# Optimization experiments

Measured on AMD Instinct MI355X. Metric: run time of the kernel, lower is better.

Reference implementation:

```python
import jax, jax.numpy as jnp
import numpy as np

N = 100_000          # total nodes across batch
E = 3_200_000        # total edges
L = 64               # token sequence length per node
VOCAB = 6
EMBED = 16
HID = 16             # gcn_hidden
EDGE_FEAT = 5
EDGE_HID = 16
NUM_GRAPHS = 64
NODE_IN = EMBED + 1  # Hseq concat x_cov


def setup_inputs() -> dict:
    key = jax.random.key(0)
    ks = jax.random.split(key, 14)
    seq_tokens = jax.random.randint(ks[0], (N, L), 0, VOCAB, dtype=jnp.int32)
    x_cov = jax.random.normal(ks[1], (N, 1), dtype=jnp.float32)
    edge_index = jax.random.randint(ks[2], (2, E), 0, N, dtype=jnp.int32)
    edge_attr = jax.random.normal(ks[3], (E, EDGE_FEAT), dtype=jnp.float32)
    batch = jnp.sort(jax.random.randint(ks[4], (N,), 0, NUM_GRAPHS, dtype=jnp.int32))
    # parameters
    embed = jax.random.normal(ks[5], (VOCAB, EMBED), dtype=jnp.float32) * 0.1
    embed = embed.at[0].set(0.0)  # padding_idx=0
    w1 = jax.random.normal(ks[6], (NODE_IN, HID), dtype=jnp.float32) * (NODE_IN ** -0.5)
    b1 = jnp.zeros((HID,), jnp.float32)
    w2 = jax.random.normal(ks[7], (HID, HID), dtype=jnp.float32) * (HID ** -0.5)
    b2 = jnp.zeros((HID,), jnp.float32)
    we1 = jax.random.normal(ks[8], (2 * HID + EDGE_FEAT, EDGE_HID), dtype=jnp.float32) * ((2 * HID + EDGE_FEAT) ** -0.5)
    be1 = jnp.zeros((EDGE_HID,), jnp.float32)
    we2 = jax.random.normal(ks[9], (EDGE_HID, 1), dtype=jnp.float32) * (EDGE_HID ** -0.5)
    be2 = jnp.zeros((1,), jnp.float32)
    return dict(seq_tokens=seq_tokens, x_cov=x_cov, edge_index=edge_index,
                edge_attr=edge_attr, batch=batch, embed=embed,
                w1=w1, b1=b1, w2=w2, b2=b2, we1=we1, be1=be1, we2=we2, be2=be2)


def reference(seq_tokens, x_cov, edge_index, edge_attr, batch,
              embed, w1, b1, w2, b2, we1, be1, we2, be2):
    # --- encode_nodes: masked mean of token embeddings + covariate ---
    Emb = embed[seq_tokens]                                   # [N, L, EMBED]
    mask = (seq_tokens != 0).astype(jnp.float32)[..., None]   # [N, L, 1]
    lengths = jnp.maximum(mask.sum(axis=1), 1.0)              # [N, 1]
    Hseq = (Emb * mask).sum(axis=1) / lengths                 # [N, EMBED]
    X = jnp.concatenate([Hseq, x_cov], axis=1)                # [N, NODE_IN]

    # --- per-graph dense GCN, expressed as equivalent block-diagonal sparse MP ---
    src, dst = edge_index[0], edge_index[1]
    valid = (batch[src] == batch[dst]).astype(jnp.float32)    # within-graph edges only
    # row-sum degree: out-degree (valid edges) + self loop + eps, per torch code
    deg = jax.ops.segment_sum(valid, src, num_segments=N) + 1.0 + 1e-8
    dinv = deg ** -0.5                                        # [N]

    def gcn(H, W, b):
        M = H @ W + b                                         # [N, HID]
        msg = (valid * dinv[dst])[:, None] * M[dst]           # [E, HID]
        agg = jax.ops.segment_sum(msg, src, num_segments=N)   # scatter-add over src
        return jax.nn.relu(dinv[:, None] * (agg + dinv[:, None] * M))

    H = gcn(X, w1, b1)
    H = gcn(H, w2, b2)

    # --- edge MLP on gathered node pairs ---
    feats = jnp.concatenate([H[src], H[dst], edge_attr], axis=1)  # [E, 2*HID+5]
    h = jax.nn.relu(feats @ we1 + be1)
    logits = (h @ we2 + be2)[:, 0]                            # [E]
    return logits
```

## Files before the change

### kernel.cpp

```cpp
#include <hip/hip_runtime.h>
#include <hip/hip_bf16.h>
#include <hip/hip_fp16.h>

#define BS 256
#define NG 64
#define VCAP 131072
#define PBUF 256

__device__ __forceinline__ uint4 pack8(const float* f) {
    union { uint4 u; __half2 h[4]; } v;
    v.h[0] = __floats2half2_rn(f[0], f[1]);
    v.h[1] = __floats2half2_rn(f[2], f[3]);
    v.h[2] = __floats2half2_rn(f[4], f[5]);
    v.h[3] = __floats2half2_rn(f[6], f[7]);
    return v.u;
}

__device__ __forceinline__ void unpack8(uint4 u, float* f) {
    const __half2* h = (const __half2*)&u;
    float2 t;
    t = __half22float2(h[0]); f[0] = t.x; f[1] = t.y;
    t = __half22float2(h[1]); f[2] = t.x; f[3] = t.y;
    t = __half22float2(h[2]); f[4] = t.x; f[5] = t.y;
    t = __half22float2(h[3]); f[6] = t.x; f[7] = t.y;
}

__global__ __launch_bounds__(BS) void encode_kernel(
        const int* __restrict__ seq,
        const float* __restrict__ xcov,
        const int* __restrict__ batch,
        const float* __restrict__ embed,
        const float* __restrict__ w1,
        const float* __restrict__ b1,
        float* __restrict__ M1,
        int* __restrict__ deg,
        int* __restrict__ tail,
        int* __restrict__ bnd, int N) {
    __shared__ float sE[96];
    __shared__ float sW1[272];
    __shared__ float sB1[16];
    __shared__ float sEW[80];
    int tid = threadIdx.x;
    for (int i = tid; i < 96; i += BS) sE[i] = embed[i];
    for (int i = tid; i < 272; i += BS) sW1[i] = w1[i];
    if (tid < 16) sB1[tid] = b1[tid];
    __syncthreads();
    if (tid < 80) {
        int t = tid >> 4, j = tid & 15;
        float a = 0.f;
#pragma unroll
        for (int k = 0; k < 16; k++) a += sE[(t + 1) * 16 + k] * sW1[k * 16 + j];
        sEW[tid] = a;
    }
    __syncthreads();

    int gid = blockIdx.x * BS + tid;
    if (gid < N) deg[gid] = 0;
    if (gid == 0) *tail = 0;

    int n = blockIdx.x * 16 + (tid >> 4);
    int j = tid & 15;
    if (n >= N) return;

    if (j == 0) {
        int b = batch[n];
        if (n == 0) {
            for (int g = 0; g <= b; g++) bnd[g] = 0;
        } else {
            int pb = batch[n - 1];
            for (int g = pb + 1; g <= b; g++) bnd[g] = n;
        }
        if (n == N - 1) {
            for (int g = b + 1; g <= NG; g++) bnd[g] = N;
        }
    }

    int4 v = ((const int4*)seq)[(size_t)n * 16 + j];
    int c1 = (v.x == 1) + (v.y == 1) + (v.z == 1) + (v.w == 1);
    int c2 = (v.x == 2) + (v.y == 2) + (v.z == 2) + (v.w == 2);
    int c3 = (v.x == 3) + (v.y == 3) + (v.z == 3) + (v.w == 3);
    int c4 = (v.x == 4) + (v.y == 4) + (v.z == 4) + (v.w == 4);
    int c5 = (v.x == 5) + (v.y == 5) + (v.z == 5) + (v.w == 5);
#pragma unroll
    for (int m = 1; m < 16; m <<= 1) {
        c1 += __shfl_xor(c1, m);
        c2 += __shfl_xor(c2, m);
        c3 += __shfl_xor(c3, m);
        c4 += __shfl_xor(c4, m);
        c5 += __shfl_xor(c5, m);
    }
    float f1 = (float)c1, f2 = (float)c2, f3 = (float)c3, f4 = (float)c4, f5 = (float)c5;
    float tot = f1 + f2 + f3 + f4 + f5;
    float inv = 1.0f / fmaxf(tot, 1.0f);
    float xc = xcov[n];
    float o = sB1[j] + xc * sW1[256 + j] +
              inv * (f1 * sEW[j] + f2 * sEW[16 + j] + f3 * sEW[32 + j] +
                     f4 * sEW[48 + j] + f5 * sEW[64 + j]);
    M1[(size_t)n * 16 + j] = o;
}

__device__ __forceinline__ int find_graph(const int* bnd, int s) {
    int g = 0;
#pragma unroll
    for (int step = 32; step; step >>= 1) {
        int c = g + step;
        if (c <= NG - 1 && bnd[c] <= s) g = c;
    }
    return g;
}

__global__ __launch_bounds__(BS) void prep_kernel(
        const int* __restrict__ ei,
        const int* __restrict__ bndg,
        int* __restrict__ deg,
        int2* __restrict__ vlist,
        int* __restrict__ tail, int E) {
    __shared__ int sBnd[NG + 1];
    __shared__ int2 sList[PBUF];
    __shared__ int sCnt;
    __shared__ int sBase;
    int tid = threadIdx.x;
    if (tid <= NG) sBnd[tid] = bndg[tid];
    if (tid == 0) sCnt = 0;
    __syncthreads();

    int idx = (blockIdx.x * BS + tid) * 4;
    if (idx + 3 < E) {
        int4 s4 = *(const int4*)(ei + idx);
        int4 d4 = *(const int4*)(ei + E + idx);
#pragma unroll
        for (int j = 0; j < 4; j++) {
            int s = (&s4.x)[j], d = (&d4.x)[j];
            int g = find_graph(sBnd, s);
            if (d >= sBnd[g] && d < sBnd[g + 1]) {
                atomicAdd(&deg[s], 1);
                int lp = atomicAdd(&sCnt, 1);
                if (lp < PBUF) sList[lp] = make_int2(s, d);
            }
        }
    } else {
        for (int j = 0; j < 4; j++) {
            int e = idx + j;
            if (e < E) {
                int s = ei[e], d = ei[E + e];
                int g = find_graph(sBnd, s);
                if (d >= sBnd[g] && d < sBnd[g + 1]) {
                    atomicAdd(&deg[s], 1);
                    int lp = atomicAdd(&sCnt, 1);
                    if (lp < PBUF) sList[lp] = make_int2(s, d);
                }
            }
        }
    }
    __syncthreads();
    if (tid == 0) {
        int c = sCnt < PBUF ? sCnt : PBUF;
        sBase = atomicAdd(tail, c);
        sCnt = c;
    }
    __syncthreads();
    int c = sCnt, b = sBase;
    for (int i = tid; i < c; i += BS) {
        int gp = b + i;
        if (gp < VCAP) vlist[gp] = sList[i];
    }
}

__global__ __launch_bounds__(BS) void scan1_kernel(
        const int* __restrict__ deg,
        int* __restrict__ off,
        int* __restrict__ bsum,
        int* __restrict__ csrD, int N) {
    __shared__ int wsum[4];
    int tid = threadIdx.x;
    int n = blockIdx.x * BS + tid;

    int stride = gridDim.x * BS;
    for (int i = blockIdx.x * BS + tid; i < VCAP; i += stride) csrD[i] = 0;

    int v = (n < N) ? deg[n] : 0;
    int lane = tid & 63, wv = tid >> 6;
    int x = v;
#pragma unroll
    for (int o = 1; o < 64; o <<= 1) {
        int y = __shfl_up(x, o);
        if (lane >= o) x += y;
    }
    if (lane == 63) wsum[wv] = x;
    __syncthreads();
    if (wv == 0 && lane < 4) {
        int w = wsum[lane];
#pragma unroll
        for (int o = 1; o < 4; o <<= 1) {
            int y = __shfl_up(w, o);
            if (lane >= o) w += y;
        }
        wsum[lane] = w;
    }
    __syncthreads();
    int base = (wv > 0) ? wsum[wv - 1] : 0;
    if (n < N) off[n] = base + x - v;
    if (tid == BS - 1) bsum[blockIdx.x] = wsum[3];
}

__global__ __launch_bounds__(64) void scan2_kernel(int* __restrict__ bsum, int nb) {
    int lane = threadIdx.x;
    int l[8];
    int s = 0;
    int base0 = lane * 8;
#pragma unroll
    for (int k = 0; k < 8; k++) {
        int i = base0 + k;
        l[k] = (i < nb) ? bsum[i] : 0;
        s += l[k];
    }
    int x = s;
#pragma unroll
    for (int o = 1; o < 64; o <<= 1) {
        int y = __shfl_up(x, o);
        if (lane >= o) x += y;
    }
    int run = x - s;
#pragma unroll
    for (int k = 0; k < 8; k++) {
        int i = base0 + k;
        if (i < nb) bsum[i] = run;
        run += l[k];
    }
}

__global__ __launch_bounds__(BS) void scan3_kernel(
        const int* __restrict__ deg,
        const int* __restrict__ off,
        const int* __restrict__ bsum,
        int2* __restrict__ OD,
        int* __restrict__ cur,
        float* __restrict__ Dinv, int N) {
    int n = blockIdx.x * BS + threadIdx.x;
    if (n >= N) return;
    int beg = off[n] + bsum[blockIdx.x];
    int dg = deg[n];
    OD[n] = make_int2(beg, dg);
    cur[n] = beg;
    Dinv[n] = 1.0f / sqrtf((float)dg + 1.0f + 1e-8f);
}

__global__ __launch_bounds__(BS) void place_kernel(
        const int2* __restrict__ vlist,
        const int* __restrict__ tail,
        int* __restrict__ cur,
        int* __restrict__ csrD) {
    int nt = *tail;
    if (nt > VCAP) nt = VCAP;
    int stride = gridDim.x * BS;
    for (int i = blockIdx.x * BS + threadIdx.x; i < nt; i += stride) {
        int2 e = vlist[i];
        int pos = atomicAdd(&cur[e.x], 1);
        if (pos < VCAP) csrD[pos] = e.y;
    }
}

__global__ __launch_bounds__(BS) void layer1_kernel(
        const int2* __restrict__ OD,
        const float* __restrict__ Dinv,
        const int* __restrict__ csrD,
        const float* __restrict__ M1,
        float* __restrict__ M2,
        const float* __restrict__ w2,
        const float* __restrict__ b2,
        int N) {
    __shared__ float sW2[256];
    __shared__ float sB2[16];
    int tid = threadIdx.x;
    for (int i = tid; i < 256; i += BS) sW2[i] = w2[i];
    if (tid < 16) sB2[tid] = b2[tid];
    __syncthreads();

    int n = blockIdx.x * BS + tid;
    if (n >= N) return;

    int2 od = OD[n];
    float di = Dinv[n];
    float acc[16];
#pragma unroll
    for (int j = 0; j < 16; j++) acc[j] = 0.f;
    int beg = od.x, end = od.x + od.y;
    if (beg > VCAP) beg = VCAP;
    if (end > VCAP) end = VCAP;
    for (int e = beg; e < end; e++) {
        int d = csrD[e];
        float dd = Dinv[d];
        const float4* m4 = (const float4*)(M1 + (size_t)d * 16);
        float4 a = m4[0], b = m4[1], c = m4[2], q = m4[3];
        acc[0] += dd * a.x; acc[1] += dd * a.y; acc[2] += dd * a.z; acc[3] += dd * a.w;
        acc[4] += dd * b.x; acc[5] += dd * b.y; acc[6] += dd * b.z; acc[7] += dd * b.w;
        acc[8] += dd * c.x; acc[9] += dd * c.y; acc[10] += dd * c.z; acc[11] += dd * c.w;
        acc[12] += dd * q.x; acc[13] += dd * q.y; acc[14] += dd * q.z; acc[15] += dd * q.w;
    }
    const float4* mr = (const float4*)(M1 + (size_t)n * 16);
    float4 m0 = mr[0], m1 = mr[1], m2 = mr[2], m3 = mr[3];
    float m[16] = {m0.x,m0.y,m0.z,m0.w, m1.x,m1.y,m1.z,m1.w,
                   m2.x,m2.y,m2.z,m2.w, m3.x,m3.y,m3.z,m3.w};
    float h[16];
#pragma unroll
    for (int j = 0; j < 16; j++) h[j] = fmaxf(di * (acc[j] + di * m[j]), 0.0f);
    float o[16];
#pragma unroll
    for (int j = 0; j < 16; j++) o[j] = sB2[j];
#pragma unroll
    for (int k = 0; k < 16; k++) {
        float hk = h[k];
#pragma unroll
        for (int j = 0; j < 16; j++) o[j] += hk * sW2[k * 16 + j];
    }
    float4* wr = (float4*)(M2 + (size_t)n * 16);
    wr[0] = make_float4(o[0], o[1], o[2], o[3]);
    wr[1] = make_float4(o[4], o[5], o[6], o[7]);
    wr[2] = make_float4(o[8], o[9], o[10], o[11]);
    wr[3] = make_float4(o[12], o[13], o[14], o[15]);
}

__global__ __launch_bounds__(BS) void layer2_kernel(
        const int2* __restrict__ OD,
        const float* __restrict__ Dinv,
        const int* __restrict__ csrD,
        const float* __restrict__ M2,
        char* __restrict__ PQ,
        const float* __restrict__ we1,
        int N) {
    __shared__ float sWe1[512];
    int tid = threadIdx.x;
    for (int i = tid; i < 512; i += BS) sWe1[i] = we1[i];
    __syncthreads();

    int n = blockIdx.x * BS + tid;
    if (n >= N) return;

    int2 od = OD[n];
    float di = Dinv[n];
    float acc[16];
#pragma unroll
    for (int j = 0; j < 16; j++) acc[j] = 0.f;
    int beg = od.x, end = od.x + od.y;
    if (beg > VCAP) beg = VCAP;
    if (end > VCAP) end = VCAP;
    for (int e = beg; e < end; e++) {
        int d = csrD[e];
        float dd = Dinv[d];
        const float4* m4 = (const float4*)(M2 + (size_t)d * 16);
        float4 a = m4[0], b = m4[1], c = m4[2], q = m4[3];
        acc[0] += dd * a.x; acc[1] += dd * a.y; acc[2] += dd * a.z; acc[3] += dd * a.w;
        acc[4] += dd * b.x; acc[5] += dd * b.y; acc[6] += dd * b.z; acc[7] += dd * b.w;
        acc[8] += dd * c.x; acc[9] += dd * c.y; acc[10] += dd * c.z; acc[11] += dd * c.w;
        acc[12] += dd * q.x; acc[13] += dd * q.y; acc[14] += dd * q.z; acc[15] += dd * q.w;
    }
    const float4* mr = (const float4*)(M2 + (size_t)n * 16);
    float4 m0 = mr[0], m1 = mr[1], m2 = mr[2], m3 = mr[3];
    float m[16] = {m0.x,m0.y,m0.z,m0.w, m1.x,m1.y,m1.z,m1.w,
                   m2.x,m2.y,m2.z,m2.w, m3.x,m3.y,m3.z,m3.w};
    float h[16];
#pragma unroll
    for (int j = 0; j < 16; j++) h[j] = fmaxf(di * (acc[j] + di * m[j]), 0.0f);
    float p[16], q[16];
#pragma unroll
    for (int j = 0; j < 16; j++) { p[j] = 0.f; q[j] = 0.f; }
#pragma unroll
    for (int k = 0; k < 16; k++) {
        float hk = h[k];
#pragma unroll
        for (int j = 0; j < 16; j++) {
            p[j] += hk * sWe1[k * 16 + j];
            q[j] += hk * sWe1[(16 + k) * 16 + j];
        }
    }
    uint4* pr = (uint4*)(PQ + (size_t)n * 64);
    pr[0] = pack8(p); pr[1] = pack8(p + 8);
    pr[2] = pack8(q); pr[3] = pack8(q + 8);
}

__device__ __forceinline__ float mlp_one(
        uint4 pa, uint4 pb, uint4 qa, uint4 qb,
        float a0, float a1, float a2, float a3, float a4,
        const float* sB, const float* sC, const float* sV, float sb2) {
    float p[16], q[16];
    unpack8(pa, p); unpack8(pb, p + 8);
    unpack8(qa, q); unpack8(qb, q + 8);
    float lg = sb2;
#pragma unroll
    for (int j = 0; j < 16; j++) {
        float acc = sB[j] + p[j] + q[j] +
                    a0 * sC[j] + a1 * sC[16 + j] + a2 * sC[32 + j] +
                    a3 * sC[48 + j] + a4 * sC[64 + j];
        lg += fmaxf(acc, 0.0f) * sV[j];
    }
    return lg;
}

__global__ __launch_bounds__(BS) void edge_mlp_kernel(
        const int* __restrict__ ei,
        const char* __restrict__ PQ,
        const float* __restrict__ eattr,
        const float* __restrict__ we1,
        const float* __restrict__ be1,
        const float* __restrict__ we2,
        const float* __restrict__ be2,
        float* __restrict__ out, int E) {
    __shared__ float sC[80];
    __shared__ float sB[16];
    __shared__ float sV[16];
    __shared__ float sb2;
    int tid = threadIdx.x;
    if (tid < 80) sC[tid] = we1[512 + tid];
    if (tid < 16) { sB[tid] = be1[tid]; sV[tid] = we2[tid]; }
    if (tid == 0) sb2 = be2[0];
    __syncthreads();

    int e0 = (blockIdx.x * BS + tid) * 4;
    if (e0 >= E) return;

    if (e0 + 3 < E) {
        int4 s4 = *(const int4*)(ei + e0);
        int4 d4 = *(const int4*)(ei + E + e0);
        const uint4* p0 = (const uint4*)(PQ + (size_t)s4.x * 64);
        const uint4* p1 = (const uint4*)(PQ + (size_t)s4.y * 64);
        const uint4* p2 = (const uint4*)(PQ + (size_t)s4.z * 64);
        const uint4* p3 = (const uint4*)(PQ + (size_t)s4.w * 64);
        const uint4* q0 = (const uint4*)(PQ + (size_t)d4.x * 64 + 32);
        const uint4* q1 = (const uint4*)(PQ + (size_t)d4.y * 64 + 32);
        const uint4* q2 = (const uint4*)(PQ + (size_t)d4.z * 64 + 32);
        const uint4* q3 = (const uint4*)(PQ + (size_t)d4.w * 64 + 32);
        uint4 pa0 = p0[0], pb0 = p0[1], qa0 = q0[0], qb0 = q0[1];
        uint4 pa1 = p1[0], pb1 = p1[1], qa1 = q1[0], qb1 = q1[1];
        uint4 pa2 = p2[0], pb2 = p2[1], qa2 = q2[0], qb2 = q2[1];
        uint4 pa3 = p3[0], pb3 = p3[1], qa3 = q3[0], qb3 = q3[1];
        const float4* at = (const float4*)(eattr + (size_t)e0 * 5);
        float4 A0 = at[0], A1 = at[1], A2 = at[2], A3 = at[3], A4 = at[4];

        float r0 = mlp_one(pa0, pb0, qa0, qb0, A0.x, A0.y, A0.z, A0.w, A1.x, sB, sC, sV, sb2);
        float r1 = mlp_one(pa1, pb1, qa1, qb1, A1.y, A1.z, A1.w, A2.x, A2.y, sB, sC, sV, sb2);
        float r2 = mlp_one(pa2, pb2, qa2, qb2, A2.z, A2.w, A3.x, A3.y, A3.z, sB, sC, sV, sb2);
        float r3 = mlp_one(pa3, pb3, qa3, qb3, A3.w, A4.x, A4.y, A4.z, A4.w, sB, sC, sV, sb2);
        *(float4*)(out + e0) = make_float4(r0, r1, r2, r3);
    } else {
        for (int j = 0; j < 4; j++) {
            int e = e0 + j;
            if (e < E) {
                int s = ei[e], d = ei[E + e];
                const uint4* pr = (const uint4*)(PQ + (size_t)s * 64);
                const uint4* qr = (const uint4*)(PQ + (size_t)d * 64 + 32);
                uint4 pa = pr[0], pb = pr[1], qa = qr[0], qb = qr[1];
                const float* ea = eattr + (size_t)e * 5;
                float lg = mlp_one(pa, pb, qa, qb, ea[0], ea[1], ea[2], ea[3], ea[4],
                                   sB, sC, sV, sb2);
                out[e] = lg;
            }
        }
    }
}

extern "C" void kernel_launch(void* const* d_in, const int* in_sizes, int n_in,
                              void* d_out, int out_size, void* d_ws, size_t ws_size,
                              hipStream_t stream) {
    const int* seq     = (const int*)d_in[0];
    const float* xcov  = (const float*)d_in[1];
    const int* ei      = (const int*)d_in[2];
    const float* eattr = (const float*)d_in[3];
    const int* batch   = (const int*)d_in[4];
    const float* embed = (const float*)d_in[5];
    const float* w1    = (const float*)d_in[6];
    const float* b1    = (const float*)d_in[7];
    const float* w2    = (const float*)d_in[8];
    const float* b2    = (const float*)d_in[9];
    const float* we1   = (const float*)d_in[10];
    const float* be1   = (const float*)d_in[11];
    const float* we2   = (const float*)d_in[12];
    const float* be2   = (const float*)d_in[13];
    float* out         = (float*)d_out;

    int N = in_sizes[1];
    int E = in_sizes[2] / 2;

    char* ws = (char*)d_ws;
    size_t off_b = 0;
    auto alloc = [&](size_t bytes) -> void* {
        void* p = ws + off_b;
        off_b += (bytes + 255) & ~(size_t)255;
        return p;
    };
    float* M1    = (float*)alloc((size_t)N * 16 * sizeof(float));
    float* M2    = (float*)alloc((size_t)N * 16 * sizeof(float));
    char* PQ     = (char*)alloc((size_t)N * 64);
    int* bndg    = (int*)alloc((NG + 1) * sizeof(int));
    int* deg     = (int*)alloc((size_t)N * sizeof(int));
    int* offA    = (int*)alloc((size_t)N * sizeof(int));
    int* cur     = (int*)alloc((size_t)N * sizeof(int));
    int2* OD     = (int2*)alloc((size_t)N * sizeof(int2));
    float* Dinv  = (float*)alloc((size_t)N * sizeof(float));
    int* bsum    = (int*)alloc(512 * sizeof(int));
    int2* vlist  = (int2*)alloc((size_t)VCAP * sizeof(int2));
    int* csrD    = (int*)alloc((size_t)VCAP * sizeof(int));
    int* tail    = (int*)alloc(16 * sizeof(int));

    int gn16 = ((size_t)N * 16 + BS - 1) / BS;
    int gp   = (E + BS * 4 - 1) / (BS * 4);
    int gs   = (N + BS - 1) / BS;
    int ge4  = (E + BS * 4 - 1) / (BS * 4);

    encode_kernel<<<gn16, BS, 0, stream>>>(seq, xcov, batch, embed, w1, b1,
                                           M1, deg, tail, bndg, N);
    prep_kernel<<<gp, BS, 0, stream>>>(ei, bndg, deg, vlist, tail, E);
    scan1_kernel<<<gs, BS, 0, stream>>>(deg, offA, bsum, csrD, N);
    scan2_kernel<<<1, 64, 0, stream>>>(bsum, gs);
    scan3_kernel<<<gs, BS, 0, stream>>>(deg, offA, bsum, OD, cur, Dinv, N);
    place_kernel<<<208, BS, 0, stream>>>(vlist, tail, cur, csrD);
    layer1_kernel<<<gs, BS, 0, stream>>>(OD, Dinv, csrD, M1, M2, w2, b2, N);
    layer2_kernel<<<gs, BS, 0, stream>>>(OD, Dinv, csrD, M2, PQ, we1, N);
    edge_mlp_kernel<<<ge4, BS, 0, stream>>>(ei, PQ, eattr, we1, be1, we2, be2, out, E);
}
```

Measured before the change: 301.3 us.

## Replace CSR build with atomic scatter aggregation and per-feature node kernels

Drops the scan and place kernels that built a CSR of valid edges. Aggregation becomes an atomic scatter-add of dinv-scaled neighbor features into zeroed accumulators A1 and A2. Node layers now run 16 threads per node and broadcast features with shuffles, and the edge MLP goes to one edge per thread with nontemporal loads. The aim is fewer launches and less serial scan work, at the cost of float atomics, extra zeroing traffic and nondeterministic summation order.

Result: faster. 290.4 us (-3.6%).

```diff
diff --git a/kernel.cpp b/kernel.cpp
--- a/kernel.cpp
+++ b/kernel.cpp
@@ -33,6 +33,8 @@
         const float* __restrict__ w1,
         const float* __restrict__ b1,
         float* __restrict__ M1,
+        float* __restrict__ A1,
+        float* __restrict__ A2,
         int* __restrict__ deg,
         int* __restrict__ tail,
         int* __restrict__ bnd, int N) {
@@ -54,8 +56,9 @@
     }
     __syncthreads();
 
-    int gid = blockIdx.x * BS + tid;
-    if (gid < N) deg[gid] = 0;
+    size_t gid = (size_t)blockIdx.x * BS + tid;
+    if (gid < (size_t)N * 16) { A1[gid] = 0.f; A2[gid] = 0.f; }
+    if (gid < (size_t)N) deg[gid] = 0;
     if (gid == 0) *tail = 0;
 
     int n = blockIdx.x * 16 + (tid >> 4);
@@ -166,109 +169,31 @@
     }
 }
 
-__global__ __launch_bounds__(BS) void scan1_kernel(
-        const int* __restrict__ deg,
-        int* __restrict__ off,
-        int* __restrict__ bsum,
-        int* __restrict__ csrD, int N) {
-    __shared__ int wsum[4];
-    int tid = threadIdx.x;
-    int n = blockIdx.x * BS + tid;
-
-    int stride = gridDim.x * BS;
-    for (int i = blockIdx.x * BS + tid; i < VCAP; i += stride) csrD[i] = 0;
-
-    int v = (n < N) ? deg[n] : 0;
-    int lane = tid & 63, wv = tid >> 6;
-    int x = v;
-#pragma unroll
-    for (int o = 1; o < 64; o <<= 1) {
-        int y = __shfl_up(x, o);
-        if (lane >= o) x += y;
-    }
-    if (lane == 63) wsum[wv] = x;
-    __syncthreads();
-    if (wv == 0 && lane < 4) {
-        int w = wsum[lane];
-#pragma unroll
-        for (int o = 1; o < 4; o <<= 1) {
-            int y = __shfl_up(w, o);
-            if (lane >= o) w += y;
-        }
-        wsum[lane] = w;
-    }
-    __syncthreads();
-    int base = (wv > 0) ? wsum[wv - 1] : 0;
-    if (n < N) off[n] = base + x - v;
-    if (tid == BS - 1) bsum[blockIdx.x] = wsum[3];
-}
-
-__global__ __launch_bounds__(64) void scan2_kernel(int* __restrict__ bsum, int nb) {
-    int lane = threadIdx.x;
-    int l[8];
-    int s = 0;
-    int base0 = lane * 8;
-#pragma unroll
-    for (int k = 0; k < 8; k++) {
-        int i = base0 + k;
-        l[k] = (i < nb) ? bsum[i] : 0;
-        s += l[k];
-    }
-    int x = s;
-#pragma unroll
-    for (int o = 1; o < 64; o <<= 1) {
-        int y = __shfl_up(x, o);
-        if (lane >= o) x += y;
-    }
-    int run = x - s;
-#pragma unroll
-    for (int k = 0; k < 8; k++) {
-        int i = base0 + k;
-        if (i < nb) bsum[i] = run;
-        run += l[k];
-    }
-}
-
-__global__ __launch_bounds__(BS) void scan3_kernel(
-        const int* __restrict__ deg,
-        const int* __restrict__ off,
-        const int* __restrict__ bsum,
-        int2* __restrict__ OD,
-        int* __restrict__ cur,
-        float* __restrict__ Dinv, int N) {
-    int n = blockIdx.x * BS + threadIdx.x;
-    if (n >= N) return;
-    int beg = off[n] + bsum[blockIdx.x];
-    int dg = deg[n];
-    OD[n] = make_int2(beg, dg);
-    cur[n] = beg;
-    Dinv[n] = 1.0f / sqrtf((float)dg + 1.0f + 1e-8f);
-}
-
-__global__ __launch_bounds__(BS) void place_kernel(
+__global__ __launch_bounds__(BS) void scatter_kernel(
         const int2* __restrict__ vlist,
         const int* __restrict__ tail,
-        int* __restrict__ cur,
-        int* __restrict__ csrD) {
+        const int* __restrict__ deg,
+        const float* __restrict__ M,
+        float* __restrict__ A) {
     int nt = *tail;
     if (nt > VCAP) nt = VCAP;
-    int stride = gridDim.x * BS;
-    for (int i = blockIdx.x * BS + threadIdx.x; i < nt; i += stride) {
+    int j = threadIdx.x & 15;
+    int estep = gridDim.x * (BS / 16);
+    for (int i = blockIdx.x * (BS / 16) + (threadIdx.x >> 4); i < nt; i += estep) {
         int2 e = vlist[i];
-        int pos = atomicAdd(&cur[e.x], 1);
-        if (pos < VCAP) csrD[pos] = e.y;
-    }
-}
-
-__global__ __launch_bounds__(BS) void layer1_kernel(
-        const int2* __restrict__ OD,
-        const float* __restrict__ Dinv,
-        const int* __restrict__ csrD,
+        float dd = 1.0f / sqrtf((float)deg[e.y] + 1.0f + 1e-8f);
+        float val = dd * M[(size_t)e.y * 16 + j];
+        atomicAdd(&A[(size_t)e.x * 16 + j], val);
+    }
+}
+
+__global__ __launch_bounds__(BS) void finish1_kernel(
+        const float* __restrict__ A1,
         const float* __restrict__ M1,
-        float* __restrict__ M2,
+        const int* __restrict__ deg,
         const float* __restrict__ w2,
         const float* __restrict__ b2,
-        int N) {
+        float* __restrict__ M2, int N) {
     __shared__ float sW2[256];
     __shared__ float sB2[16];
     int tid = threadIdx.x;
@@ -276,124 +201,58 @@
     if (tid < 16) sB2[tid] = b2[tid];
     __syncthreads();
 
-    int n = blockIdx.x * BS + tid;
+    int n = blockIdx.x * 16 + (tid >> 4);
+    int j = tid & 15;
     if (n >= N) return;
 
-    int2 od = OD[n];
-    float di = Dinv[n];
-    float acc[16];
-#pragma unroll
-    for (int j = 0; j < 16; j++) acc[j] = 0.f;
-    int beg = od.x, end = od.x + od.y;
-    if (beg > VCAP) beg = VCAP;
-    if (end > VCAP) end = VCAP;
-    for (int e = beg; e < end; e++) {
-        int d = csrD[e];
-        float dd = Dinv[d];
-        const float4* m4 = (const float4*)(M1 + (size_t)d * 16);
-        float4 a = m4[0], b = m4[1], c = m4[2], q = m4[3];
-        acc[0] += dd * a.x; acc[1] += dd * a.y; acc[2] += dd * a.z; acc[3] += dd * a.w;
-        acc[4] += dd * b.x; acc[5] += dd * b.y; acc[6] += dd * b.z; acc[7] += dd * b.w;
-        acc[8] += dd * c.x; acc[9] += dd * c.y; acc[10] += dd * c.z; acc[11] += dd * c.w;
-        acc[12] += dd * q.x; acc[13] += dd * q.y; acc[14] += dd * q.z; acc[15] += dd * q.w;
-    }
-    const float4* mr = (const float4*)(M1 + (size_t)n * 16);
-    float4 m0 = mr[0], m1 = mr[1], m2 = mr[2], m3 = mr[3];
-    float m[16] = {m0.x,m0.y,m0.z,m0.w, m1.x,m1.y,m1.z,m1.w,
-                   m2.x,m2.y,m2.z,m2.w, m3.x,m3.y,m3.z,m3.w};
-    float h[16];
-#pragma unroll
-    for (int j = 0; j < 16; j++) h[j] = fmaxf(di * (acc[j] + di * m[j]), 0.0f);
-    float o[16];
-#pragma unroll
-    for (int j = 0; j < 16; j++) o[j] = sB2[j];
+    float di = 1.0f / sqrtf((float)deg[n] + 1.0f + 1e-8f);
+    size_t base = (size_t)n * 16;
+    float a = A1[base + j];
+    float m = M1[base + j];
+    float h = fmaxf(di * (a + di * m), 0.0f);
+
+    int lb = (tid & 63) & 48;
+    float o = sB2[j];
 #pragma unroll
     for (int k = 0; k < 16; k++) {
-        float hk = h[k];
-#pragma unroll
-        for (int j = 0; j < 16; j++) o[j] += hk * sW2[k * 16 + j];
-    }
-    float4* wr = (float4*)(M2 + (size_t)n * 16);
-    wr[0] = make_float4(o[0], o[1], o[2], o[3]);
-    wr[1] = make_float4(o[4], o[5], o[6], o[7]);
-    wr[2] = make_float4(o[8], o[9], o[10], o[11]);
-    wr[3] = make_float4(o[12], o[13], o[14], o[15]);
-}
-
-__global__ __launch_bounds__(BS) void layer2_kernel(
-        const int2* __restrict__ OD,
-        const float* __restrict__ Dinv,
-        const int* __restrict__ csrD,
+        float hk = __shfl(h, lb + k);
+        o += hk * sW2[k * 16 + j];
+    }
+    M2[base + j] = o;
+}
+
+__global__ __launch_bounds__(BS) void finish2_kernel(
+        const float* __restrict__ A2,
         const float* __restrict__ M2,
-        char* __restrict__ PQ,
+        const int* __restrict__ deg,
         const float* __restrict__ we1,
-        int N) {
+        char* __restrict__ PQ, int N) {
     __shared__ float sWe1[512];
     int tid = threadIdx.x;
     for (int i = tid; i < 512; i += BS) sWe1[i] = we1[i];
     __syncthreads();
 
-    int n = blockIdx.x * BS + tid;
+    int n = blockIdx.x * 16 + (tid >> 4);
+    int j = tid & 15;
     if (n >= N) return;
 
-    int2 od = OD[n];
-    float di = Dinv[n];
-    float acc[16];
-#pragma unroll
-    for (int j = 0; j < 16; j++) acc[j] = 0.f;
-    int beg = od.x, end = od.x + od.y;
-    if (beg > VCAP) beg = VCAP;
-    if (end > VCAP) end = VCAP;
-    for (int e = beg; e < end; e++) {
-        int d = csrD[e];
-        float dd = Dinv[d];
-        const float4* m4 = (const float4*)(M2 + (size_t)d * 16);
-        float4 a = m4[0], b = m4[1], c = m4[2], q = m4[3];
-        acc[0] += dd * a.x; acc[1] += dd * a.y; acc[2] += dd * a.z; acc[3] += dd * a.w;
-        acc[4] += dd * b.x; acc[5] += dd * b.y; acc[6] += dd * b.z; acc[7] += dd * b.w;
-        acc[8] += dd * c.x; acc[9] += dd * c.y; acc[10] += dd * c.z; acc[11] += dd * c.w;
-        acc[12] += dd * q.x; acc[13] += dd * q.y; acc[14] += dd * q.z; acc[15] += dd * q.w;
-    }
-    const float4* mr = (const float4*)(M2 + (size_t)n * 16);
-    float4 m0 = mr[0], m1 = mr[1], m2 = mr[2], m3 = mr[3];
-    float m[16] = {m0.x,m0.y,m0.z,m0.w, m1.x,m1.y,m1.z,m1.w,
-                   m2.x,m2.y,m2.z,m2.w, m3.x,m3.y,m3.z,m3.w};
-    float h[16];
-#pragma unroll
-    for (int j = 0; j < 16; j++) h[j] = fmaxf(di * (acc[j] + di * m[j]), 0.0f);
-    float p[16], q[16];
-#pragma unroll
-    for (int j = 0; j < 16; j++) { p[j] = 0.f; q[j] = 0.f; }
+    float di = 1.0f / sqrtf((float)deg[n] + 1.0f + 1e-8f);
+    size_t base = (size_t)n * 16;
+    float a = A2[base + j];
+    float m = M2[base + j];
+    float h = fmaxf(di * (a + di * m), 0.0f);
+
+    int lb = (tid & 63) & 48;
+    float p = 0.f, q = 0.f;
 #pragma unroll
     for (int k = 0; k < 16; k++) {
-        float hk = h[k];
-#pragma unroll
-        for (int j = 0; j < 16; j++) {
-            p[j] += hk * sWe1[k * 16 + j];
-            q[j] += hk * sWe1[(16 + k) * 16 + j];
-        }
-    }
-    uint4* pr = (uint4*)(PQ + (size_t)n * 64);
-    pr[0] = pack8(p); pr[1] = pack8(p + 8);
-    pr[2] = pack8(q); pr[3] = pack8(q + 8);
-}
-
-__device__ __forceinline__ float mlp_one(
-        uint4 pa, uint4 pb, uint4 qa, uint4 qb,
-        float a0, float a1, float a2, float a3, float a4,
-        const float* sB, const float* sC, const float* sV, float sb2) {
-    float p[16], q[16];
-    unpack8(pa, p); unpack8(pb, p + 8);
-    unpack8(qa, q); unpack8(qb, q + 8);
-    float lg = sb2;
-#pragma unroll
-    for (int j = 0; j < 16; j++) {
-        float acc = sB[j] + p[j] + q[j] +
-                    a0 * sC[j] + a1 * sC[16 + j] + a2 * sC[32 + j] +
-                    a3 * sC[48 + j] + a4 * sC[64 + j];
-        lg += fmaxf(acc, 0.0f) * sV[j];
-    }
-    return lg;
+        float hk = __shfl(h, lb + k);
+        p += hk * sWe1[k * 16 + j];
+        q += hk * sWe1[(16 + k) * 16 + j];
+    }
+    __half* row = (__half*)(PQ + (size_t)n * 64);
+    row[j] = __float2half(p);
+    row[16 + j] = __float2half(q);
 }
 
 __global__ __launch_bounds__(BS) void edge_mlp_kernel(
@@ -414,48 +273,34 @@
     if (tid < 16) { sB[tid] = be1[tid]; sV[tid] = we2[tid]; }
     if (tid == 0) sb2 = be2[0];
     __syncthreads();
-
-    int e0 = (blockIdx.x * BS + tid) * 4;
-    if (e0 >= E) return;
-
-    if (e0 + 3 < E) {
-        int4 s4 = *(const int4*)(ei + e0);
-        int4 d4 = *(const int4*)(ei + E + e0);
-        const uint4* p0 = (const uint4*)(PQ + (size_t)s4.x * 64);
-        const uint4* p1 = (const uint4*)(PQ + (size_t)s4.y * 64);
-        const uint4* p2 = (const uint4*)(PQ + (size_t)s4.z * 64);
-        const uint4* p3 = (const uint4*)(PQ + (size_t)s4.w * 64);
-        const uint4* q0 = (const uint4*)(PQ + (size_t)d4.x * 64 + 32);
-        const uint4* q1 = (const uint4*)(PQ + (size_t)d4.y * 64 + 32);
-        const uint4* q2 = (const uint4*)(PQ + (size_t)d4.z * 64 + 32);
-        const uint4* q3 = (const uint4*)(PQ + (size_t)d4.w * 64 + 32);
-        uint4 pa0 = p0[0], pb0 = p0[1], qa0 = q0[0], qb0 = q0[1];
-        uint4 pa1 = p1[0], pb1 = p1[1], qa1 = q1[0], qb1 = q1[1];
-        uint4 pa2 = p2[0], pb2 = p2[1], qa2 = q2[0], qb2 = q2[1];
-        uint4 pa3 = p3[0], pb3 = p3[1], qa3 = q3[0], qb3 = q3[1];
-        const float4* at = (const float4*)(eattr + (size_t)e0 * 5);
-        float4 A0 = at[0], A1 = at[1], A2 = at[2], A3 = at[3], A4 = at[4];
-
-        float r0 = mlp_one(pa0, pb0, qa0, qb0, A0.x, A0.y, A0.z, A0.w, A1.x, sB, sC, sV, sb2);
-        float r1 = mlp_one(pa1, pb1, qa1, qb1, A1.y, A1.z, A1.w, A2.x, A2.y, sB, sC, sV, sb2);
-        float r2 = mlp_one(pa2, pb2, qa2, qb2, A2.z, A2.w, A3.x, A3.y, A3.z, sB, sC, sV, sb2);
-        float r3 = mlp_one(pa3, pb3, qa3, qb3, A3.w, A4.x, A4.y, A4.z, A4.w, sB, sC, sV, sb2);
-        *(float4*)(out + e0) = make_float4(r0, r1, r2, r3);
-    } else {
-        for (int j = 0; j < 4; j++) {
-            int e = e0 + j;
-            if (e < E) {
-                int s = ei[e], d = ei[E + e];
-                const uint4* pr = (const uint4*)(PQ + (size_t)s * 64);
-                const uint4* qr = (const uint4*)(PQ + (size_t)d * 64 + 32);
-                uint4 pa = pr[0], pb = pr[1], qa = qr[0], qb = qr[1];
-                const float* ea = eattr + (size_t)e * 5;
-                float lg = mlp_one(pa, pb, qa, qb, ea[0], ea[1], ea[2], ea[3], ea[4],
-                                   sB, sC, sV, sb2);
-                out[e] = lg;
-            }
-        }
-    }
+    int e = blockIdx.x * BS + tid;
+    if (e >= E) return;
+    int s = __builtin_nontemporal_load(ei + e);
+    int d = __builtin_nontemporal_load(ei + E + e);
+    const uint4* pr = (const uint4*)(PQ + (size_t)s * 64);
+    const uint4* qr = (const uint4*)(PQ + (size_t)d * 64 + 32);
+    uint4 pa = pr[0], pb = pr[1];
+    uint4 qa = qr[0], qb = qr[1];
+    const float* ea = eattr + (size_t)e * 5;
+    float a0 = __builtin_nontemporal_load(ea + 0);
+    float a1 = __builtin_nontemporal_load(ea + 1);
+    float a2 = __builtin_nontemporal_load(ea + 2);
+    float a3 = __builtin_nontemporal_load(ea + 3);
+    float a4 = __builtin_nontemporal_load(ea + 4);
+
+    float p[16], q[16];
+    unpack8(pa, p); unpack8(pb, p + 8);
+    unpack8(qa, q); unpack8(qb, q + 8);
+
+    float lg = sb2;
+#pragma unroll
+    for (int j = 0; j < 16; j++) {
+        float acc = sB[j] + p[j] + q[j] +
+                    a0 * sC[j] + a1 * sC[16 + j] + a2 * sC[32 + j] +
+                    a3 * sC[48 + j] + a4 * sC[64 + j];
+        lg += fmaxf(acc, 0.0f) * sV[j];
+    }
+    __builtin_nontemporal_store(lg, out + e);
 }
 
 extern "C" void kernel_launch(void* const* d_in, const int* in_sizes, int n_in,
@@ -489,31 +334,24 @@
     };
     float* M1    = (float*)alloc((size_t)N * 16 * sizeof(float));
     float* M2    = (float*)alloc((size_t)N * 16 * sizeof(float));
+    float* A1    = (float*)alloc((size_t)N * 16 * sizeof(float));
+    float* A2    = (float*)alloc((size_t)N * 16 * sizeof(float));
     char* PQ     = (char*)alloc((size_t)N * 64);
     int* bndg    = (int*)alloc((NG + 1) * sizeof(int));
     int* deg     = (int*)alloc((size_t)N * sizeof(int));
-    int* offA    = (int*)alloc((size_t)N * sizeof(int));
-    int* cur     = (int*)alloc((size_t)N * sizeof(int));
-    int2* OD     = (int2*)alloc((size_t)N * sizeof(int2));
-    float* Dinv  = (float*)alloc((size_t)N * sizeof(float));
-    int* bsum    = (int*)alloc(512 * sizeof(int));
     int2* vlist  = (int2*)alloc((size_t)VCAP * sizeof(int2));
-    int* csrD    = (int*)alloc((size_t)VCAP * sizeof(int));
     int* tail    = (int*)alloc(16 * sizeof(int));
 
-    int gn16 = ((size_t)N * 16 + BS - 1) / BS;
+    int gn16 = (int)(((size_t)N * 16 + BS - 1) / BS);
     int gp   = (E + BS * 4 - 1) / (BS * 4);
-    int gs   = (N + BS - 1) / BS;
-    int ge4  = (E + BS * 4 - 1) / (BS * 4);
+    int ge   = (E + BS - 1) / BS;
 
     encode_kernel<<<gn16, BS, 0, stream>>>(seq, xcov, batch, embed, w1, b1,
-                                           M1, deg, tail, bndg, N);
+                                           M1, A1, A2, deg, tail, bndg, N);
     prep_kernel<<<gp, BS, 0, stream>>>(ei, bndg, deg, vlist, tail, E);
-    scan1_kernel<<<gs, BS, 0, stream>>>(deg, offA, bsum, csrD, N);
-    scan2_kernel<<<1, 64, 0, stream>>>(bsum, gs);
-    scan3_kernel<<<gs, BS, 0, stream>>>(deg, offA, bsum, OD, cur, Dinv, N);
-    place_kernel<<<208, BS, 0, stream>>>(vlist, tail, cur, csrD);
-    layer1_kernel<<<gs, BS, 0, stream>>>(OD, Dinv, csrD, M1, M2, w2, b2, N);
-    layer2_kernel<<<gs, BS, 0, stream>>>(OD, Dinv, csrD, M2, PQ, we1, N);
-    edge_mlp_kernel<<<ge4, BS, 0, stream>>>(ei, PQ, eattr, we1, be1, we2, be2, out, E);
-}
+    scatter_kernel<<<1024, BS, 0, stream>>>(vlist, tail, deg, M1, A1);
+    finish1_kernel<<<gn16, BS, 0, stream>>>(A1, M1, deg, w2, b2, M2, N);
+    scatter_kernel<<<1024, BS, 0, stream>>>(vlist, tail, deg, M2, A2);
+    finish2_kernel<<<gn16, BS, 0, stream>>>(A2, M2, deg, we1, PQ, N);
+    edge_mlp_kernel<<<ge, BS, 0, stream>>>(ei, PQ, eattr, we1, be1, we2, be2, out, E);
+}
```
